# Performance work log

Hardware: AMD Instinct MI355X
Metric: run time of the kernel (lower is better)

## Reference

```python
import jax, jax.numpy as jnp
import numpy as np

N_CHAINS = 4
CHAIN_LEN = 512
N = N_CHAINS * CHAIN_LEN          # 2048 residues
H = 128                           # h_channels
FC = 3                            # frame_channels
CIN = H + FC                      # fused sphere channels (131)
NH = 8                            # attention heads
VD = H // 4                       # attn value channels per head
NCOEF = 4                         # lmax=1 -> (lmax+1)^2 coefficients
KNN_K = 30
LR_K = 10
NEG = jnp.float32(-1e30)

BB_IDEAL = np.array([[-0.525, 1.363, 0.0], [0.0, 0.0, 0.0], [1.526, 0.0, 0.0]], np.float32)  # N, CA, C ideal coords


def _safe_norm(v, keepdims=False):
    return jnp.sqrt(jnp.sum(v * v, axis=-1, keepdims=keepdims) + 1e-12)


def _normalize(v):
    return v / _safe_norm(v, keepdims=True)


def _edge_rot_mat(vec):
    # deterministic orthonormal frame with first row along the edge direction
    x = _normalize(vec)
    ref = jnp.where(jnp.abs(x[..., :1]) > 0.99,
                    jnp.array([0.0, 1.0, 0.0], x.dtype),
                    jnp.array([1.0, 0.0, 0.0], x.dtype))
    z = _normalize(jnp.cross(x, ref))
    y = jnp.cross(z, x)
    return jnp.stack([x, y, z], axis=-2)          # [E,3,3]


def _rbf(d, d_min=0.0, d_max=20.0, n=16):
    mu = jnp.linspace(d_min, d_max, n)
    sigma = (d_max - d_min) / n
    return jnp.exp(-(((d[..., None] - mu) / sigma) ** 2))


def _relpos(edge_index, n=16):
    d = (edge_index[0] - edge_index[1]).astype(jnp.float32)
    freq = jnp.exp(jnp.arange(0, n, 2, dtype=jnp.float32) * (-np.log(10000.0) / n))
    ang = d[:, None] * freq
    return jnp.concatenate([jnp.cos(ang), jnp.sin(ang)], axis=-1)


def _quat_to_rot(q):
    w, x, y, z = q[..., 0], q[..., 1], q[..., 2], q[..., 3]
    r0 = jnp.stack([1 - 2 * (y * y + z * z), 2 * (x * y - w * z), 2 * (x * z + w * y)], -1)
    r1 = jnp.stack([2 * (x * y + w * z), 1 - 2 * (x * x + z * z), 2 * (y * z - w * x)], -1)
    r2 = jnp.stack([2 * (x * z - w * y), 2 * (y * z + w * x), 1 - 2 * (x * x + y * y)], -1)
    return jnp.stack([r0, r1, r2], -2)


def _build_edges(trans, batch, seq_local_edge_index):
    d2 = jnp.sum((trans[:, None] - trans[None]) ** 2, -1)   # [N,N]
    same = batch[:, None] == batch[None]
    eye = jnp.eye(N, dtype=bool)
    d2m = jnp.where(same & ~eye, d2, jnp.float32(1e30))
    _, knn_idx = jax.lax.top_k(-d2m, KNN_K)                 # kNN neighbors
    g = jax.random.gumbel(jax.random.key(42), d2m.shape)
    _, lr_idx = jax.lax.top_k(-1.5 * jnp.log(d2m) + g, LR_K)  # inv-cubic sampling p ~ d^-3
    src = jnp.concatenate([knn_idx.reshape(-1), lr_idx.reshape(-1), seq_local_edge_index[0]])
    dst = jnp.concatenate([jnp.repeat(jnp.arange(N), KNN_K), jnp.repeat(jnp.arange(N), LR_K), seq_local_edge_index[1]])
    return jnp.stack([src, dst])


def _forward(rots, trans, node_features, Wa1, ba1, Wa2, Wv, Wo, Wg, Wf1, Wf2, Wr1, br1, Wr2, br2, Wr3, br3, Wt, batch, x_mask, noising_mask, seq_local_edge_index):
    edge_index = _build_edges(trans, batch, seq_local_edge_index)
    src, dst = edge_index[0], edge_index[1]
    vec = trans[src] - trans[dst]
    dist = _safe_norm(vec)
    valid = jnp.isfinite(dist) & (dist > 1e-3)              # edge_select mask (kept static-shape)
    R = _edge_rot_mat(vec)                                  # [E,3,3] per-edge Wigner (l=1)
    ef = jnp.concatenate([_rbf(dist), _relpos(edge_index)], -1)  # [E,32]
    # fuse node embedding with backbone frame atoms and editability flag
    bb_atoms = jnp.einsum('nij,aj->nai', rots, jnp.asarray(BB_IDEAL)) + trans[:, None]  # [N,3atoms,3]
    fused = jnp.zeros((N, NCOEF, CIN), node_features.dtype)
    fused = fused.at[:, :, :H].set(node_features)
    fused = fused.at[:, 1:4, H:].set(jnp.swapaxes(bb_atoms, -1, -2))
    editable = noising_mask & (~x_mask)
    fused = fused.at[:, 0, -1].set(editable.astype(fused.dtype))
    # SO3-equivariant attention (TransBlockV2)
    x0 = fused[:, 0]                                        # invariant l=0 features [N,CIN]
    a_in = jnp.concatenate([x0[src], x0[dst], ef], -1)      # [E, 2*CIN+32]
    logits = jax.nn.leaky_relu(a_in @ Wa1 + ba1) @ Wa2      # [E,NH]
    logits = jnp.where(valid[:, None], logits, NEG)
    m = jax.ops.segment_max(logits, dst, num_segments=N)
    m = jnp.where(m > NEG / 2, m, 0.0)
    p = jnp.where(valid[:, None], jnp.exp(logits - m[dst]), 0.0)
    z = jax.ops.segment_sum(p, dst, num_segments=N)
    attn = p / (z[dst] + 1e-9)                              # segment softmax over incoming edges
    xs = fused[src]
    xs = xs.at[:, 1:4].set(jnp.einsum('eij,ejc->eic', R, xs[:, 1:4]))  # rotate l=1 into edge frame
    v = (xs @ Wv).reshape(xs.shape[0], NCOEF, NH, VD)
    msg = (attn[:, None, :, None] * v).reshape(xs.shape[0], NCOEF, NH * VD)
    msg = msg.at[:, 1:4].set(jnp.einsum('eji,ejc->eic', R, msg[:, 1:4]))  # rotate back (R^T)
    agg = jax.ops.segment_sum(msg, dst, num_segments=N)     # [N,4,NH*VD]
    out = agg @ Wo                                          # [N,4,H]
    # gated equivariant FFN
    y0 = out[:, 0]
    gate = jax.nn.sigmoid(y0 @ Wg)
    f0 = jax.nn.relu(y0 @ Wf1) @ Wf2
    bb_update = jnp.concatenate([(y0 + f0)[:, None], out[:, 1:4] * gate[:, None, :]], axis=1)
    # frame rotation update from invariants
    inv = bb_update[:, 0]
    h1 = jax.nn.relu(inv @ Wr1 + br1)
    h2 = jax.nn.relu(h1 @ Wr2 + br2)
    qv = (h2 @ Wr3 + br3)[:, :3]
    quat = jnp.concatenate([jnp.ones_like(qv[:, :1]), qv], -1)
    quat = quat / jnp.linalg.norm(quat, axis=-1, keepdims=True)
    rot_update = _quat_to_rot(quat)
    # equivariant translation update (SO3_LinearV2 on l=1)
    trans_update = (bb_update[:, 1:4] @ Wt)[..., 0]         # [N,3]
    rots_new = jnp.where(noising_mask[:, None, None], jnp.einsum('nij,njk->nik', rots, rot_update), rots)
    trans_new = jnp.where(noising_mask[:, None], trans + trans_update, trans)
    return rots_new, trans_new, bb_update


def setup_inputs():
    key = jax.random.key(0)
    ks = jax.random.split(key, 20)
    q = jax.random.normal(ks[0], (N, 4))
    q = q / jnp.linalg.norm(q, axis=-1, keepdims=True)
    rots = _quat_to_rot(q)                                  # proper rotation matrices
    trans = jax.random.normal(ks[1], (N, 3)) * 10.0
    node_features = jax.random.normal(ks[2], (N, NCOEF, H)) * 0.1
    batch = jnp.repeat(jnp.arange(N_CHAINS), CHAIN_LEN)
    x_mask = jax.random.bernoulli(ks[3], 0.1, (N,))
    noising_mask = jax.random.bernoulli(ks[4], 0.5, (N,))
    idx = jnp.arange(N)
    nxt = jnp.where((idx + 1) % CHAIN_LEN == 0, idx, idx + 1)
    seq_local_edge_index = jnp.stack([jnp.concatenate([idx, nxt]), jnp.concatenate([nxt, idx])])

    def lin(k, i, o):
        return jax.random.normal(k, (i, o)) / np.sqrt(i)

    AIN = 2 * CIN + 32
    return dict(
        rots=rots, trans=trans, node_features=node_features,
        Wa1=lin(ks[5], AIN, H), ba1=jnp.zeros((H,)),
        Wa2=lin(ks[6], H, NH),
        Wv=lin(ks[7], CIN, NH * VD),
        Wo=lin(ks[8], NH * VD, H),
        Wg=lin(ks[9], H, H), Wf1=lin(ks[10], H, H), Wf2=lin(ks[11], H, H),
        Wr1=lin(ks[12], H, 2 * H), br1=jnp.zeros((2 * H,)),
        Wr2=lin(ks[13], 2 * H, H), br2=jnp.zeros((H,)),
        Wr3=lin(ks[14], H, 6), br3=jnp.zeros((6,)),
        Wt=lin(ks[15], H, 1),
        batch=batch, x_mask=x_mask, noising_mask=noising_mask,
        seq_local_edge_index=seq_local_edge_index)


def reference(rots, trans, node_features, Wa1, ba1, Wa2, Wv, Wo, Wg, Wf1, Wf2, Wr1, br1, Wr2, br2, Wr3, br3, Wt, batch, x_mask, noising_mask, seq_local_edge_index):
    return _forward(rots, trans, node_features, Wa1, ba1, Wa2, Wv, Wo, Wg, Wf1, Wf2, Wr1, br1, Wr2, br2, Wr3, br3, Wt, batch, x_mask, noising_mask, seq_local_edge_index)
```

## Files before the change

kernel.cpp:

```cpp
#include <hip/hip_runtime.h>
#include <hip/hip_bf16.h>
#include <math.h>

#define NN 2048
#define CHAIN 512
#define KNN 30
#define LRK 10
#define NFIX 40
#define NSLOT 42
#define HPAD 132
#define AGPAD 260
#define NREL 1023

#define OUT_ROT 0
#define OUT_TRANS (NN*9)
#define OUT_BB (NN*9 + NN*3)

#define THREEFRY_PARTITIONABLE 1

__device__ __forceinline__ int xcd_swz(int b){ return ((b & 7) << 8) | (b >> 3); }

__device__ __forceinline__ unsigned rotl32(unsigned x, unsigned r){ return (x<<r)|(x>>(32u-r)); }

__device__ __forceinline__ void tf_block(unsigned &x0, unsigned &x1){
  const unsigned k0 = 0u, k1 = 42u, k2 = 0x1BD11BDAu ^ 0u ^ 42u;
  x0 += k0; x1 += k1;
#define TFR(a) x0 += x1; x1 = rotl32(x1,(a)); x1 ^= x0;
  TFR(13) TFR(15) TFR(26) TFR(6)   x0 += k1; x1 += k2 + 1u;
  TFR(17) TFR(29) TFR(16) TFR(24)  x0 += k2; x1 += k0 + 2u;
  TFR(13) TFR(15) TFR(26) TFR(6)   x0 += k0; x1 += k1 + 3u;
  TFR(17) TFR(29) TFR(16) TFR(24)  x0 += k1; x1 += k2 + 4u;
  TFR(13) TFR(15) TFR(26) TFR(6)   x0 += k2; x1 += k0 + 5u;
#undef TFR
}

__device__ __forceinline__ float gumbel_from_bits(unsigned bits){
  float f = __uint_as_float((bits >> 9) | 0x3f800000u) - 1.0f;
  const float tiny = 1.17549435e-38f;
  float u = fmaxf(tiny, f * (1.0f - tiny) + tiny);
  return -logf(-logf(u));
}

__device__ __forceinline__ float gumbel_at(unsigned p){
#if THREEFRY_PARTITIONABLE
  unsigned x0 = 0u, x1 = p;
  tf_block(x0, x1);
  return gumbel_from_bits(x0 ^ x1);
#else
  const unsigned HALF = (NN*(unsigned)NN)/2u;
  unsigned c0, c1; bool lo = p < HALF;
  if(lo){ c0 = p; c1 = p + HALF; } else { c0 = p - HALF; c1 = p; }
  tf_block(c0, c1);
  return gumbel_from_bits(lo ? c0 : c1);
#endif
}

__global__ __launch_bounds__(256) void k_pretop(
    const float* __restrict__ rots, const float* __restrict__ trans,
    const float* __restrict__ nf, const float* __restrict__ Wa1,
    const float* __restrict__ Wv,
    const int* __restrict__ xmask, const int* __restrict__ nmask,
    float* __restrict__ P, float* __restrict__ U, float* __restrict__ V,
    int* __restrict__ srcs, float* __restrict__ Trel)
{
  __shared__ __align__(16) char smem[4*4*132*4];
  int bb = blockIdx.x, t = threadIdx.x;

  if(bb >= NN + 512){
    int r = (bb - (NN+512))*2 + (t >> 7);
    int k = t & 127;
    if(r < NREL){
      float rel = (float)(r - 511);
      float acc = 0.f;
#pragma unroll
      for(int j=0;j<8;j++){
        float fr = expf((float)(2*j) * (float)(-0.5756462732485115));
        float ang = rel * fr;
        acc += cosf(ang) * Wa1[(278+j)*128 + k];
        acc += sinf(ang) * Wa1[(286+j)*128 + k];
      }
      Trel[r*128 + k] = acc;
    }
    return;
  }

  if(bb < NN){
    unsigned* s_kk = (unsigned*)smem;
    unsigned* s_lk = s_kk + CHAIN;
    int i = bb;
    int base = (i >> 9) << 9;
    float tx = trans[i*3+0], ty = trans[i*3+1], tz = trans[i*3+2];
    for(int q=t; q<CHAIN; q+=256){
      int j = base + q;
      float dx = __fsub_rn(trans[j*3+0], tx);
      float dy = __fsub_rn(trans[j*3+1], ty);
      float dz = __fsub_rn(trans[j*3+2], tz);
      float d2 = __fadd_rn(__fadd_rn(__fmul_rn(dx,dx),__fmul_rn(dy,dy)),__fmul_rn(dz,dz));
      bool val = (j != i);
      float dm = val ? d2 : 1e30f;
      s_kk[q] = __float_as_uint(dm) ^ 0x80000000u;
      if(val){
        float g = gumbel_at((unsigned)(i*NN + j));
        float sc = __fadd_rn(__fmul_rn(-1.5f, logf(dm)), g);
        unsigned b = __float_as_uint(sc);
        unsigned ord = b ^ ((b & 0x80000000u) ? 0xFFFFFFFFu : 0x80000000u);
        s_lk[q] = ~ord;
      } else {
        s_lk[q] = 0xFFFFFFFFu;
      }
    }
    __syncthreads();
    if(t < 128){
      int w = t >> 6, lane = t & 63;
      unsigned* arr = w ? s_lk : s_kk;
      int K = w ? LRK : KNN;
      int outoff = w ? KNN : 0;
      unsigned long long best = ~0ull;
      for(int q=lane; q<CHAIN; q+=64){
        unsigned long long kk = ((unsigned long long)arr[q]<<32) | (unsigned)q;
        if(kk < best) best = kk;
      }
      for(int k=0;k<K;k++){
        unsigned long long r = best;
        for(int off=32; off; off>>=1){
          unsigned long long o = __shfl_xor(r, off, 64);
          if(o < r) r = o;
        }
        int winq = (int)(unsigned)(r & 0xffffffffull);
        if(lane == 0){
          srcs[i*NFIX + outoff + k] = base + winq;
          arr[winq] = 0xFFFFFFFFu;
        }
        asm volatile("s_waitcnt lgkmcnt(0)" ::: "memory");
        __builtin_amdgcn_wave_barrier();
        if((winq & 63) == lane){
          best = ~0ull;
          for(int q=lane; q<CHAIN; q+=64){
            unsigned long long kk = ((unsigned long long)arr[q]<<32) | (unsigned)q;
            if(kk < best) best = kk;
          }
        }
      }
    }
    return;
  }

  float (*fr)[4][132] = (float (*)[4][132])smem;
  int n0 = (bb - NN)*4;
  for(int i=t; i<2048; i+=256){
    int nd = i>>9, c = (i>>7)&3, kk = i&127;
    fr[nd][c][kk] = nf[(n0+nd)*512 + c*128 + kk];
  }
  if(t < 4){
    fr[t][0][128] = 0.0f; fr[t][0][129] = 0.0f;
    fr[t][0][130] = (nmask[n0+t] != 0 && xmask[n0+t] == 0) ? 1.0f : 0.0f;
  } else if(t >= 16 && t < 52){
    int q = t - 16; int nd = q/9, r = q%9, a = r/3, i = r%3;
    int n = n0 + nd;
    const float BB[3][3] = {{-0.525f,1.363f,0.0f},{0.f,0.f,0.f},{1.526f,0.f,0.f}};
    float bb_ = rots[n*9+i*3+0]*BB[a][0] + rots[n*9+i*3+1]*BB[a][1]
              + rots[n*9+i*3+2]*BB[a][2] + trans[n*3+i];
    fr[nd][1+i][128+a] = bb_;
  }
  __syncthreads();

  float a[4][4];
#pragma unroll
  for(int nd=0;nd<4;nd++)
#pragma unroll
    for(int c=0;c<4;c++) a[nd][c]=0.f;
  for(int j=0;j<128;j+=4){
    float w0=Wv[(j+0)*256+t], w1=Wv[(j+1)*256+t], w2=Wv[(j+2)*256+t], w3=Wv[(j+3)*256+t];
#pragma unroll
    for(int nd=0;nd<4;nd++){
#pragma unroll
      for(int c=0;c<4;c++){
        float4 f4 = *(const float4*)&fr[nd][c][j];
        a[nd][c] += f4.x*w0 + f4.y*w1 + f4.z*w2 + f4.w*w3;
      }
    }
  }
  for(int j=128;j<131;j++){
    float w = Wv[j*256+t];
#pragma unroll
    for(int nd=0;nd<4;nd++)
#pragma unroll
      for(int c=0;c<4;c++) a[nd][c] += fr[nd][c][j]*w;
  }
#pragma unroll
  for(int nd=0;nd<4;nd++){
    float4 v4; v4.x=a[nd][0]; v4.y=a[nd][1]; v4.z=a[nd][2]; v4.w=a[nd][3];
    *(float4*)&P[(n0+nd)*1024 + t*4] = v4;
  }

  int k = t & 127;
  int isV = t >> 7;
  const float* Wcol = Wa1 + (isV ? 131*128 : 0);
  float u[4] = {0.f,0.f,0.f,0.f};
  for(int j=0;j<128;j+=4){
    float w0=Wcol[(j+0)*128+k], w1=Wcol[(j+1)*128+k], w2=Wcol[(j+2)*128+k], w3=Wcol[(j+3)*128+k];
#pragma unroll
    for(int nd=0;nd<4;nd++){
      float4 f4 = *(const float4*)&fr[nd][0][j];
      u[nd] += f4.x*w0 + f4.y*w1 + f4.z*w2 + f4.w*w3;
    }
  }
  for(int j=128;j<131;j++){
    float w = Wcol[j*128+k];
#pragma unroll
    for(int nd=0;nd<4;nd++) u[nd] += fr[nd][0][j]*w;
  }
  float* OUT = isV ? V : U;
#pragma unroll
  for(int nd=0;nd<4;nd++) OUT[(n0+nd)*128 + k] = u[nd];
}

__global__ __launch_bounds__(256) void k_attn(
    const float* __restrict__ trans, const float* __restrict__ Wa1,
    const float* __restrict__ ba1, const float* __restrict__ Wa2,
    const float* __restrict__ Wo,
    const float* __restrict__ U, const float* __restrict__ V,
    const float* __restrict__ P, const float* __restrict__ Trel,
    const int* __restrict__ srcs, float* __restrict__ Y)
{
  __shared__ int   s_src[NSLOT];
  __shared__ int   s_val[NSLOT];
  __shared__ float s_dist[NSLOT];
  __shared__ __align__(16) float s_H[NSLOT*HPAD];
  __shared__ __align__(16) float s_mux[NSLOT*32];
  __shared__ float s_att[NSLOT*8];

  int b = blockIdx.x, t = threadIdx.x;
  int d = xcd_swz(b);
  int pos = d & (CHAIN-1);
  int k = t & 127, grp = t >> 7;

  if(t < NSLOT){
    int src;
    if(t < NFIX)      src = srcs[d*NFIX + t];
    else if(t == NFIX) src = (pos > 0)       ? d-1 : d;
    else               src = (pos < CHAIN-1) ? d+1 : d;
    s_src[t] = src;
    float dx = trans[src*3+0]-trans[d*3+0];
    float dy = trans[src*3+1]-trans[d*3+1];
    float dz = trans[src*3+2]-trans[d*3+2];
    float dist = sqrtf(dx*dx + dy*dy + dz*dz + 1e-12f);
    s_dist[t] = dist;
    s_val[t] = (dist > 1e-3f) ? 1 : 0;
  }

  float wreg[16];
#pragma unroll
  for(int f=0; f<16; f++) wreg[f] = Wa1[(262+f)*128 + k];
  float ubias = ba1[k] + V[d*128 + k];
  __syncthreads();

  for(int i=t; i<NSLOT*16; i+=256){
    int e = i >> 4, f = i & 15;
    float zz = (s_dist[e] - (float)f * (20.0f/15.0f)) * 0.8f;
    s_mux[i] = expf(-(zz*zz));
  }
  __syncthreads();

  for(int e = grp; e < NSLOT; e += 2){
    int src = s_src[e];
    s_H[e*HPAD + k] = U[src*128 + k] + Trel[(src - d + 511)*128 + k];
  }
  for(int e = grp; e < NSLOT; e += 2){
    float h = ubias + s_H[e*HPAD + k];
    const float4* rp = (const float4*)(s_mux + e*16);
#pragma unroll
    for(int q=0; q<4; q++){
      float4 ev = rp[q];
      h += ev.x*wreg[4*q+0] + ev.y*wreg[4*q+1] + ev.z*wreg[4*q+2] + ev.w*wreg[4*q+3];
    }
    h = (h >= 0.0f) ? h : 0.01f*h;
    s_H[e*HPAD + k] = h;
  }
  __syncthreads();

  for(int i=t; i<1024; i+=256){
    int kk = i >> 3, h = i & 7;
    s_mux[h*HPAD + kk] = Wa2[i];
  }
  __syncthreads();

  for(int p = t; p < NSLOT*8; p += 256){
    int e = p >> 3, h = p & 7;
    const float4* Hp = (const float4*)(s_H + e*HPAD);
    const float4* Wp = (const float4*)(s_mux + h*HPAD);
    float acc = 0.f;
#pragma unroll
    for(int q=0; q<32; q++){
      float4 a = Hp[q], w = Wp[q];
      acc += a.x*w.x + a.y*w.y + a.z*w.z + a.w*w.w;
    }
    s_att[p] = s_val[e] ? acc : -1e30f;
  }
  __syncthreads();

  if(t < 64){
    int h = t & 7, g = t >> 3;
    float m = -INFINITY;
    for(int e=g; e<NSLOT; e+=8) m = fmaxf(m, s_att[e*8+h]);
    for(int off=8; off<64; off<<=1) m = fmaxf(m, __shfl_xor(m, off, 64));
    m = (m > -5e29f) ? m : 0.0f;
    float z = 0.0f;
    for(int e=g; e<NSLOT; e+=8){
      float p = expf(s_att[e*8+h] - m);
      s_att[e*8+h] = p; z += p;
    }
    for(int off=8; off<64; off<<=1) z += __shfl_xor(z, off, 64);
    float inv = 1.0f / (z + 1e-9f);
    for(int e=g; e<NSLOT; e+=8) s_att[e*8+h] *= inv;
  }
  __syncthreads();

  {
    int h = t >> 5;
    float a0=0.f,a1=0.f,a2=0.f,a3=0.f;
    for(int e=0;e<NSLOT;e++){
      float w = s_att[e*8 + h];
      float4 p4 = *(const float4*)(P + (size_t)s_src[e]*1024 + t*4);
      a0 += w*p4.x; a1 += w*p4.y; a2 += w*p4.z; a3 += w*p4.w;
    }
    s_mux[0*AGPAD + t] = a0;
    s_mux[1*AGPAD + t] = a1;
    s_mux[2*AGPAD + t] = a2;
    s_mux[3*AGPAD + t] = a3;
  }
  __syncthreads();

  {
    int cp = grp*2;
    const float* g0 = s_mux + cp*AGPAD;
    const float* g1 = s_mux + (cp+1)*AGPAD;
    float x0=0.f, x1=0.f;
    for(int u=0; u<256; u+=4){
      float w0=Wo[(u+0)*128+k], w1=Wo[(u+1)*128+k], w2=Wo[(u+2)*128+k], w3=Wo[(u+3)*128+k];
      float4 a0 = *(const float4*)(g0 + u);
      float4 a1 = *(const float4*)(g1 + u);
      x0 += a0.x*w0 + a0.y*w1 + a0.z*w2 + a0.w*w3;
      x1 += a1.x*w0 + a1.y*w1 + a1.z*w2 + a1.w*w3;
    }
    Y[d*512 + cp*128 + k]     = x0;
    Y[d*512 + (cp+1)*128 + k] = x1;
  }
}

__global__ __launch_bounds__(256) void k_node(
    const float* __restrict__ rots, const float* __restrict__ trans,
    const float* __restrict__ Y,
    const float* __restrict__ Wg, const float* __restrict__ Wf1,
    const float* __restrict__ Wf2, const float* __restrict__ Wr1,
    const float* __restrict__ br1, const float* __restrict__ Wr2,
    const float* __restrict__ br2, const float* __restrict__ Wr3,
    const float* __restrict__ br3, const float* __restrict__ Wt,
    const int* __restrict__ nmask, float* __restrict__ out)
{
  __shared__ __align__(16) float s_y[4][4][128];
  __shared__ __align__(16) float s_t1[4][128];
  __shared__ __align__(16) float s_bb0[4][128];
  __shared__ __align__(16) float s_gv[4][3][128];
  __shared__ __align__(16) float s_h1[4][256];
  __shared__ __align__(16) float s_h2[4][128];
  __shared__ float s_sc[4][8];

  int b = blockIdx.x, t = threadIdx.x;
  int half = t >> 7, k = t & 127;
  int nb = half*2;
  int dbase = b*4;
  for(int i=t; i<4*512; i+=256){
    int nd = i>>9, c=(i>>7)&3, kk=i&127;
    s_y[nd][c][kk] = Y[(dbase+nd)*512 + c*128 + kk];
  }
  __syncthreads();

  float g[2]={0.f,0.f}, f1[2]={0.f,0.f};
  for(int j=0;j<128;j+=4){
    float wg0=Wg[(j+0)*128+k], wg1=Wg[(j+1)*128+k], wg2=Wg[(j+2)*128+k], wg3=Wg[(j+3)*128+k];
    float wf0=Wf1[(j+0)*128+k], wf1_=Wf1[(j+1)*128+k], wf2_=Wf1[(j+2)*128+k], wf3=Wf1[(j+3)*128+k];
#pragma unroll
    for(int nn=0;nn<2;nn++){
      float4 yv = *(const float4*)&s_y[nb+nn][0][j];
      g[nn]  += yv.x*wg0 + yv.y*wg1 + yv.z*wg2 + yv.w*wg3;
      f1[nn] += yv.x*wf0 + yv.y*wf1_ + yv.z*wf2_ + yv.w*wf3;
    }
  }
  float gate[2];
#pragma unroll
  for(int nn=0;nn<2;nn++){
    gate[nn] = 1.0f/(1.0f + expf(-g[nn]));
    s_t1[nb+nn][k] = fmaxf(f1[nn], 0.0f);
  }
  __syncthreads();

  float f0[2]={0.f,0.f};
  for(int j=0;j<128;j+=4){
    float w0=Wf2[(j+0)*128+k], w1=Wf2[(j+1)*128+k], w2=Wf2[(j+2)*128+k], w3=Wf2[(j+3)*128+k];
#pragma unroll
    for(int nn=0;nn<2;nn++){
      float4 tv = *(const float4*)&s_t1[nb+nn][j];
      f0[nn] += tv.x*w0 + tv.y*w1 + tv.z*w2 + tv.w*w3;
    }
  }
#pragma unroll
  for(int nn=0;nn<2;nn++){
    int d = dbase + nb + nn;
    float bb0 = s_y[nb+nn][0][k] + f0[nn];
    s_bb0[nb+nn][k] = bb0;
    out[OUT_BB + d*512 + k] = bb0;
#pragma unroll
    for(int c=1;c<4;c++){
      float v = s_y[nb+nn][c][k] * gate[nn];
      s_gv[nb+nn][c-1][k] = v;
      out[OUT_BB + d*512 + c*128 + k] = v;
    }
  }
  __syncthreads();

  float a1[2], a2[2];
  a1[0]=a1[1]=br1[k]; a2[0]=a2[1]=br1[128+k];
  for(int j=0;j<128;j+=4){
    float w10=Wr1[(j+0)*256+k],     w11=Wr1[(j+1)*256+k],     w12=Wr1[(j+2)*256+k],     w13=Wr1[(j+3)*256+k];
    float w20=Wr1[(j+0)*256+128+k], w21=Wr1[(j+1)*256+128+k], w22=Wr1[(j+2)*256+128+k], w23=Wr1[(j+3)*256+128+k];
#pragma unroll
    for(int nn=0;nn<2;nn++){
      float4 bv = *(const float4*)&s_bb0[nb+nn][j];
      a1[nn] += bv.x*w10 + bv.y*w11 + bv.z*w12 + bv.w*w13;
      a2[nn] += bv.x*w20 + bv.y*w21 + bv.z*w22 + bv.w*w23;
    }
  }
#pragma unroll
  for(int nn=0;nn<2;nn++){
    s_h1[nb+nn][k] = fmaxf(a1[nn], 0.0f);
    s_h1[nb+nn][128+k] = fmaxf(a2[nn], 0.0f);
  }
  __syncthreads();

  float a[2]; a[0]=a[1]=br2[k];
  for(int j=0;j<256;j+=4){
    float w0=Wr2[(j+0)*128+k], w1=Wr2[(j+1)*128+k], w2=Wr2[(j+2)*128+k], w3=Wr2[(j+3)*128+k];
#pragma unroll
    for(int nn=0;nn<2;nn++){
      float4 hv = *(const float4*)&s_h1[nb+nn][j];
      a[nn] += hv.x*w0 + hv.y*w1 + hv.z*w2 + hv.w*w3;
    }
  }
#pragma unroll
  for(int nn=0;nn<2;nn++) s_h2[nb+nn][k] = fmaxf(a[nn], 0.0f);
  __syncthreads();

  if(t < 12){
    int nd = t/3, r = t%3;
    float q = br3[r];
    for(int kk=0;kk<128;kk++) q += s_h2[nd][kk] * Wr3[kk*6 + r];
    s_sc[nd][r] = q;
  } else if(t >= 32 && t < 44){
    int q2 = t-32; int nd = q2/3, i = q2%3;
    float s = 0.f;
    for(int kk=0;kk<128;kk++) s += s_gv[nd][i][kk] * Wt[kk];
    s_sc[nd][4+i] = s;
  }
  __syncthreads();

  if(t < 4){
    int d = dbase + t;
    int nz = nmask[d];
    float q1=s_sc[t][0], q2=s_sc[t][1], q3=s_sc[t][2];
    float nrm = sqrtf(1.0f + q1*q1 + q2*q2 + q3*q3);
    float w=1.0f/nrm, x=q1/nrm, y=q2/nrm, z=q3/nrm;
    float Ru[3][3];
    Ru[0][0]=1.f-2.f*(y*y+z*z); Ru[0][1]=2.f*(x*y-w*z);     Ru[0][2]=2.f*(x*z+w*y);
    Ru[1][0]=2.f*(x*y+w*z);     Ru[1][1]=1.f-2.f*(x*x+z*z); Ru[1][2]=2.f*(y*z-w*x);
    Ru[2][0]=2.f*(x*z-w*y);     Ru[2][1]=2.f*(y*z+w*x);     Ru[2][2]=1.f-2.f*(x*x+y*y);
    for(int i=0;i<3;i++){
      for(int j=0;j<3;j++){
        float rv;
        if(nz){
          rv = rots[d*9+i*3+0]*Ru[0][j] + rots[d*9+i*3+1]*Ru[1][j] + rots[d*9+i*3+2]*Ru[2][j];
        } else {
          rv = rots[d*9+i*3+j];
        }
        out[OUT_ROT + d*9 + i*3 + j] = rv;
      }
      float tv = trans[d*3+i];
      out[OUT_TRANS + d*3 + i] = nz ? (tv + s_sc[t][4+i]) : tv;
    }
  }
}

extern "C" void kernel_launch(void* const* d_in, const int* in_sizes, int n_in,
                              void* d_out, int out_size, void* d_ws, size_t ws_size,
                              hipStream_t stream)
{
  (void)in_sizes; (void)n_in; (void)out_size; (void)ws_size;
  const float* rots = (const float*)d_in[0];
  const float* trans = (const float*)d_in[1];
  const float* nf   = (const float*)d_in[2];
  const float* Wa1  = (const float*)d_in[3];
  const float* ba1  = (const float*)d_in[4];
  const float* Wa2  = (const float*)d_in[5];
  const float* Wv   = (const float*)d_in[6];
  const float* Wo   = (const float*)d_in[7];
  const float* Wg   = (const float*)d_in[8];
  const float* Wf1  = (const float*)d_in[9];
  const float* Wf2  = (const float*)d_in[10];
  const float* Wr1  = (const float*)d_in[11];
  const float* br1  = (const float*)d_in[12];
  const float* Wr2  = (const float*)d_in[13];
  const float* br2  = (const float*)d_in[14];
  const float* Wr3  = (const float*)d_in[15];
  const float* br3  = (const float*)d_in[16];
  const float* Wt   = (const float*)d_in[17];
  const int* xmask  = (const int*)d_in[19];
  const int* nmask  = (const int*)d_in[20];

  float* P = (float*)d_ws;
  float* U = P + NN*1024;
  float* V = U + NN*128;
  int* srcs = (int*)(V + NN*128);
  float* Y  = (float*)(srcs + NN*NFIX);
  float* Trel = Y + NN*512;

  k_pretop<<<NN + 512 + 512, 256, 0, stream>>>(rots, trans, nf, Wa1, Wv,
                                               xmask, nmask, P, U, V, srcs, Trel);
  k_attn<<<NN, 256, 0, stream>>>(trans, Wa1, ba1, Wa2, Wo, U, V, P, Trel, srcs, Y);
  k_node<<<NN/4, 256, 0, stream>>>(rots, trans, Y, Wg, Wf1, Wf2,
                                   Wr1, br1, Wr2, br2, Wr3, br3, Wt,
                                   nmask, (float*)d_out);
}
```

Measured before the change: 142.3 us.

## Keep top-k candidates in registers and widen node kernel to one node per thread group

The kNN/long-range top-k selection now keeps each lane's eight candidate keys in registers and updates only the winning lane's local minimum. This replaces the shared-memory invalidation write, the waitcnt and wave barrier, and the rescan of LDS on every round. Separately, the node MLP kernel moves from 256 to 512 threads, so each 128-thread group handles one node instead of two. That gives more parallelism per block, but the weight loads are no longer shared across two nodes per thread.

After: 139.8 us. About the same (-1.8%).

```diff
diff --git a/kernel.cpp b/kernel.cpp
--- a/kernel.cpp
+++ b/kernel.cpp
@@ -115,30 +115,41 @@
       unsigned* arr = w ? s_lk : s_kk;
       int K = w ? LRK : KNN;
       int outoff = w ? KNN : 0;
-      unsigned long long best = ~0ull;
-      for(int q=lane; q<CHAIN; q+=64){
-        unsigned long long kk = ((unsigned long long)arr[q]<<32) | (unsigned)q;
-        if(kk < best) best = kk;
+      unsigned long long k0_ = ((unsigned long long)arr[lane      ]<<32) | (unsigned)(lane);
+      unsigned long long k1_ = ((unsigned long long)arr[lane + 64 ]<<32) | (unsigned)(lane+64);
+      unsigned long long k2_ = ((unsigned long long)arr[lane + 128]<<32) | (unsigned)(lane+128);
+      unsigned long long k3_ = ((unsigned long long)arr[lane + 192]<<32) | (unsigned)(lane+192);
+      unsigned long long k4_ = ((unsigned long long)arr[lane + 256]<<32) | (unsigned)(lane+256);
+      unsigned long long k5_ = ((unsigned long long)arr[lane + 320]<<32) | (unsigned)(lane+320);
+      unsigned long long k6_ = ((unsigned long long)arr[lane + 384]<<32) | (unsigned)(lane+384);
+      unsigned long long k7_ = ((unsigned long long)arr[lane + 448]<<32) | (unsigned)(lane+448);
+      unsigned long long lmin;
+      {
+        unsigned long long a01 = k0_<k1_?k0_:k1_, a23 = k2_<k3_?k2_:k3_;
+        unsigned long long a45 = k4_<k5_?k4_:k5_, a67 = k6_<k7_?k6_:k7_;
+        unsigned long long a03 = a01<a23?a01:a23, a47 = a45<a67?a45:a67;
+        lmin = a03<a47?a03:a47;
       }
       for(int k=0;k<K;k++){
-        unsigned long long r = best;
+        unsigned long long r = lmin;
         for(int off=32; off; off>>=1){
           unsigned long long o = __shfl_xor(r, off, 64);
           if(o < r) r = o;
         }
-        int winq = (int)(unsigned)(r & 0xffffffffull);
-        if(lane == 0){
-          srcs[i*NFIX + outoff + k] = base + winq;
-          arr[winq] = 0xFFFFFFFFu;
-        }
-        asm volatile("s_waitcnt lgkmcnt(0)" ::: "memory");
-        __builtin_amdgcn_wave_barrier();
-        if((winq & 63) == lane){
-          best = ~0ull;
-          for(int q=lane; q<CHAIN; q+=64){
-            unsigned long long kk = ((unsigned long long)arr[q]<<32) | (unsigned)q;
-            if(kk < best) best = kk;
-          }
+        if(lane == 0) srcs[i*NFIX + outoff + k] = base + (int)(unsigned)(r & 0xffffffffull);
+        if(r == lmin){
+          if(k0_ == r) k0_ = ~0ull;
+          if(k1_ == r) k1_ = ~0ull;
+          if(k2_ == r) k2_ = ~0ull;
+          if(k3_ == r) k3_ = ~0ull;
+          if(k4_ == r) k4_ = ~0ull;
+          if(k5_ == r) k5_ = ~0ull;
+          if(k6_ == r) k6_ = ~0ull;
+          if(k7_ == r) k7_ = ~0ull;
+          unsigned long long a01 = k0_<k1_?k0_:k1_, a23 = k2_<k3_?k2_:k3_;
+          unsigned long long a45 = k4_<k5_?k4_:k5_, a67 = k6_<k7_?k6_:k7_;
+          unsigned long long a03 = a01<a23?a01:a23, a47 = a45<a67?a45:a67;
+          lmin = a03<a47?a03:a47;
         }
       }
     }
@@ -348,7 +359,7 @@
   }
 }
 
-__global__ __launch_bounds__(256) void k_node(
+__global__ __launch_bounds__(512) void k_node(
     const float* __restrict__ rots, const float* __restrict__ trans,
     const float* __restrict__ Y,
     const float* __restrict__ Wg, const float* __restrict__ Wf1,
@@ -367,106 +378,83 @@
   __shared__ float s_sc[4][8];
 
   int b = blockIdx.x, t = threadIdx.x;
-  int half = t >> 7, k = t & 127;
-  int nb = half*2;
+  int nd = t >> 7, k = t & 127;
   int dbase = b*4;
-  for(int i=t; i<4*512; i+=256){
-    int nd = i>>9, c=(i>>7)&3, kk=i&127;
-    s_y[nd][c][kk] = Y[(dbase+nd)*512 + c*128 + kk];
-  }
-  __syncthreads();
-
-  float g[2]={0.f,0.f}, f1[2]={0.f,0.f};
+  int d = dbase + nd;
+  for(int i=t; i<4*512; i+=512){
+    int n2 = i>>9, c=(i>>7)&3, kk=i&127;
+    s_y[n2][c][kk] = Y[(dbase+n2)*512 + c*128 + kk];
+  }
+  __syncthreads();
+
+  float g=0.f, f1=0.f;
   for(int j=0;j<128;j+=4){
     float wg0=Wg[(j+0)*128+k], wg1=Wg[(j+1)*128+k], wg2=Wg[(j+2)*128+k], wg3=Wg[(j+3)*128+k];
     float wf0=Wf1[(j+0)*128+k], wf1_=Wf1[(j+1)*128+k], wf2_=Wf1[(j+2)*128+k], wf3=Wf1[(j+3)*128+k];
-#pragma unroll
-    for(int nn=0;nn<2;nn++){
-      float4 yv = *(const float4*)&s_y[nb+nn][0][j];
-      g[nn]  += yv.x*wg0 + yv.y*wg1 + yv.z*wg2 + yv.w*wg3;
-      f1[nn] += yv.x*wf0 + yv.y*wf1_ + yv.z*wf2_ + yv.w*wf3;
-    }
-  }
-  float gate[2];
-#pragma unroll
-  for(int nn=0;nn<2;nn++){
-    gate[nn] = 1.0f/(1.0f + expf(-g[nn]));
-    s_t1[nb+nn][k] = fmaxf(f1[nn], 0.0f);
-  }
-  __syncthreads();
-
-  float f0[2]={0.f,0.f};
+    float4 yv = *(const float4*)&s_y[nd][0][j];
+    g  += yv.x*wg0 + yv.y*wg1 + yv.z*wg2 + yv.w*wg3;
+    f1 += yv.x*wf0 + yv.y*wf1_ + yv.z*wf2_ + yv.w*wf3;
+  }
+  float gate = 1.0f/(1.0f + expf(-g));
+  s_t1[nd][k] = fmaxf(f1, 0.0f);
+  __syncthreads();
+
+  float f0=0.f;
   for(int j=0;j<128;j+=4){
     float w0=Wf2[(j+0)*128+k], w1=Wf2[(j+1)*128+k], w2=Wf2[(j+2)*128+k], w3=Wf2[(j+3)*128+k];
-#pragma unroll
-    for(int nn=0;nn<2;nn++){
-      float4 tv = *(const float4*)&s_t1[nb+nn][j];
-      f0[nn] += tv.x*w0 + tv.y*w1 + tv.z*w2 + tv.w*w3;
-    }
-  }
-#pragma unroll
-  for(int nn=0;nn<2;nn++){
-    int d = dbase + nb + nn;
-    float bb0 = s_y[nb+nn][0][k] + f0[nn];
-    s_bb0[nb+nn][k] = bb0;
+    float4 tv = *(const float4*)&s_t1[nd][j];
+    f0 += tv.x*w0 + tv.y*w1 + tv.z*w2 + tv.w*w3;
+  }
+  {
+    float bb0 = s_y[nd][0][k] + f0;
+    s_bb0[nd][k] = bb0;
     out[OUT_BB + d*512 + k] = bb0;
 #pragma unroll
     for(int c=1;c<4;c++){
-      float v = s_y[nb+nn][c][k] * gate[nn];
-      s_gv[nb+nn][c-1][k] = v;
+      float v = s_y[nd][c][k] * gate;
+      s_gv[nd][c-1][k] = v;
       out[OUT_BB + d*512 + c*128 + k] = v;
     }
   }
   __syncthreads();
 
-  float a1[2], a2[2];
-  a1[0]=a1[1]=br1[k]; a2[0]=a2[1]=br1[128+k];
+  float a1 = br1[k], a2 = br1[128+k];
   for(int j=0;j<128;j+=4){
     float w10=Wr1[(j+0)*256+k],     w11=Wr1[(j+1)*256+k],     w12=Wr1[(j+2)*256+k],     w13=Wr1[(j+3)*256+k];
     float w20=Wr1[(j+0)*256+128+k], w21=Wr1[(j+1)*256+128+k], w22=Wr1[(j+2)*256+128+k], w23=Wr1[(j+3)*256+128+k];
-#pragma unroll
-    for(int nn=0;nn<2;nn++){
-      float4 bv = *(const float4*)&s_bb0[nb+nn][j];
-      a1[nn] += bv.x*w10 + bv.y*w11 + bv.z*w12 + bv.w*w13;
-      a2[nn] += bv.x*w20 + bv.y*w21 + bv.z*w22 + bv.w*w23;
-    }
-  }
-#pragma unroll
-  for(int nn=0;nn<2;nn++){
-    s_h1[nb+nn][k] = fmaxf(a1[nn], 0.0f);
-    s_h1[nb+nn][128+k] = fmaxf(a2[nn], 0.0f);
-  }
-  __syncthreads();
-
-  float a[2]; a[0]=a[1]=br2[k];
+    float4 bv = *(const float4*)&s_bb0[nd][j];
+    a1 += bv.x*w10 + bv.y*w11 + bv.z*w12 + bv.w*w13;
+    a2 += bv.x*w20 + bv.y*w21 + bv.z*w22 + bv.w*w23;
+  }
+  s_h1[nd][k] = fmaxf(a1, 0.0f);
+  s_h1[nd][128+k] = fmaxf(a2, 0.0f);
+  __syncthreads();
+
+  float a = br2[k];
   for(int j=0;j<256;j+=4){
     float w0=Wr2[(j+0)*128+k], w1=Wr2[(j+1)*128+k], w2=Wr2[(j+2)*128+k], w3=Wr2[(j+3)*128+k];
-#pragma unroll
-    for(int nn=0;nn<2;nn++){
-      float4 hv = *(const float4*)&s_h1[nb+nn][j];
-      a[nn] += hv.x*w0 + hv.y*w1 + hv.z*w2 + hv.w*w3;
-    }
-  }
-#pragma unroll
-  for(int nn=0;nn<2;nn++) s_h2[nb+nn][k] = fmaxf(a[nn], 0.0f);
+    float4 hv = *(const float4*)&s_h1[nd][j];
+    a += hv.x*w0 + hv.y*w1 + hv.z*w2 + hv.w*w3;
+  }
+  s_h2[nd][k] = fmaxf(a, 0.0f);
   __syncthreads();
 
   if(t < 12){
-    int nd = t/3, r = t%3;
+    int n2 = t/3, r = t%3;
     float q = br3[r];
-    for(int kk=0;kk<128;kk++) q += s_h2[nd][kk] * Wr3[kk*6 + r];
-    s_sc[nd][r] = q;
+    for(int kk=0;kk<128;kk++) q += s_h2[n2][kk] * Wr3[kk*6 + r];
+    s_sc[n2][r] = q;
   } else if(t >= 32 && t < 44){
-    int q2 = t-32; int nd = q2/3, i = q2%3;
+    int q2 = t-32; int n2 = q2/3, i = q2%3;
     float s = 0.f;
-    for(int kk=0;kk<128;kk++) s += s_gv[nd][i][kk] * Wt[kk];
-    s_sc[nd][4+i] = s;
+    for(int kk=0;kk<128;kk++) s += s_gv[n2][i][kk] * Wt[kk];
+    s_sc[n2][4+i] = s;
   }
   __syncthreads();
 
   if(t < 4){
-    int d = dbase + t;
-    int nz = nmask[d];
+    int d2 = dbase + t;
+    int nz = nmask[d2];
     float q1=s_sc[t][0], q2=s_sc[t][1], q3=s_sc[t][2];
     float nrm = sqrtf(1.0f + q1*q1 + q2*q2 + q3*q3);
     float w=1.0f/nrm, x=q1/nrm, y=q2/nrm, z=q3/nrm;
@@ -478,14 +466,14 @@
       for(int j=0;j<3;j++){
         float rv;
         if(nz){
-          rv = rots[d*9+i*3+0]*Ru[0][j] + rots[d*9+i*3+1]*Ru[1][j] + rots[d*9+i*3+2]*Ru[2][j];
+          rv = rots[d2*9+i*3+0]*Ru[0][j] + rots[d2*9+i*3+1]*Ru[1][j] + rots[d2*9+i*3+2]*Ru[2][j];
         } else {
-          rv = rots[d*9+i*3+j];
+          rv = rots[d2*9+i*3+j];
         }
-        out[OUT_ROT + d*9 + i*3 + j] = rv;
+        out[OUT_ROT + d2*9 + i*3 + j] = rv;
       }
-      float tv = trans[d*3+i];
-      out[OUT_TRANS + d*3 + i] = nz ? (tv + s_sc[t][4+i]) : tv;
+      float tv = trans[d2*3+i];
+      out[OUT_TRANS + d2*3 + i] = nz ? (tv + s_sc[t][4+i]) : tv;
     }
   }
 }
@@ -526,7 +514,7 @@
   k_pretop<<<NN + 512 + 512, 256, 0, stream>>>(rots, trans, nf, Wa1, Wv,
                                                xmask, nmask, P, U, V, srcs, Trel);
   k_attn<<<NN, 256, 0, stream>>>(trans, Wa1, ba1, Wa2, Wo, U, V, P, Trel, srcs, Y);
-  k_node<<<NN/4, 256, 0, stream>>>(rots, trans, Y, Wg, Wf1, Wf2,
+  k_node<<<NN/4, 512, 0, stream>>>(rots, trans, Y, Wg, Wf1, Wf2,
                                    Wr1, br1, Wr2, br2, Wr3, br3, Wt,
                                    nmask, (float*)d_out);
 }
```
